# Kernel tuning notes

Hardware: AMD Instinct MI355X
Metric: run time of the kernel (lower is better)

Reference implementation:

```python
import jax, jax.numpy as jnp
import numpy as np

N = 4096          # residues
D = 256           # local feature dim
FACTOR = 2
H = 8             # global heads
DF = D * FACTOR   # 512
DH = DF // H      # 64 per-head dim
NUM_CHAINS = 64
NUM_BATCHES = 8


def index_mean(x, idx, mask, num_segments):
    """Masked segment mean, gathered back to per-element shape.
    x: [N, ...], idx: [N] int, mask: broadcastable to x (0/1)."""
    m = mask.astype(x.dtype)
    xm = x * m
    s = jax.ops.segment_sum(xm, idx, num_segments=num_segments)
    c = jax.ops.segment_sum(jnp.broadcast_to(m, x.shape), idx, num_segments=num_segments)
    mean = s / jnp.maximum(c, 1e-6)
    return mean[idx]


def setup_inputs() -> dict:
    key = jax.random.key(0)
    ks = jax.random.split(key, 12)
    s_in = 1.0 / np.sqrt(D)
    s_mid = 1.0 / np.sqrt(2 * DF)
    return {
        "local": jax.random.normal(ks[0], (N, D), jnp.float32),
        "chain": jax.random.randint(ks[1], (N,), 0, NUM_CHAINS),
        "batch": jax.random.randint(ks[2], (N,), 0, NUM_BATCHES),
        "mask": jax.random.bernoulli(ks[3], 0.9, (N,)),
        "W_key": jax.random.normal(ks[4], (D, DF), jnp.float32) * s_in,
        "b_key": jnp.zeros((DF,), jnp.float32),
        "W_value": jax.random.normal(ks[5], (D, DF), jnp.float32) * s_in,
        "b_value": jnp.zeros((DF,), jnp.float32),
        "W_query": jax.random.normal(ks[6], (D, DF), jnp.float32) * s_in,
        "b_query": jnp.zeros((DF,), jnp.float32),
        "W_bias": jax.random.normal(ks[7], (D, 2 * DF), jnp.float32) * s_in,
        "b_bias": jnp.zeros((2 * DF,), jnp.float32),
        "W_out": jax.random.normal(ks[8], (2 * DF, D), jnp.float32) * s_mid,
    }


def reference(local, chain, batch, mask,
              W_key, b_key, W_value, b_value, W_query, b_query,
              W_bias, b_bias, W_out):
    n = local.shape[0]
    k = jax.nn.gelu(local @ W_key + b_key).reshape(n, H, DH)
    v = (local @ W_value + b_value).reshape(n, H, DH)
    q = jax.nn.gelu(local @ W_query + b_query).reshape(n, H, DH)

    bias = index_mean(local @ W_bias + b_bias, batch, mask[:, None], NUM_BATCHES)

    # outer product key (x) value: [N, H, DH, DH]
    ov = k[:, :, :, None] * v[:, :, None, :]
    m4 = mask[:, None, None, None]
    chain_op = index_mean(ov, chain, m4, NUM_CHAINS)
    batch_op = index_mean(ov, batch, m4, NUM_BATCHES)
    operation = jnp.concatenate((chain_op, batch_op), axis=-2)  # [N, H, 2*DH, DH]

    out = jnp.einsum('bhvk,bhk->bhv', operation, q).reshape(n, -1) + bias
    return out @ W_out
```

## Files before the change

kernel.cpp:

```cpp
#include <hip/hip_runtime.h>
#include <math.h>

#define NN 4096
#define DD 256
#define DFF 512
#define HH 8
#define DHH 64
#define CAP_C 256
#define CAP_B 1024

#define OFF_KB     0
#define OFF_VB     1048576
#define OFF_QB     2097152
#define OFF_ATTNB  3145728
#define OFF_STC    5242880
#define OFF_STB    7340032
#define OFF_BSUM   7602176
#define OFF_CNT    7610368
#define OFF_WQKVT  7610624
#define OFF_WOUTT  7807232
#define OFF_LISTS  7938304
#define OFF_LPART  7987456

typedef __attribute__((ext_vector_type(8))) short bf16x8;
typedef __attribute__((ext_vector_type(4))) float floatx4;

__device__ __forceinline__ float gelu_f(float x) {
    const float c = 0.7978845608028654f;
    float t = tanhf(c * (x + 0.044715f * x * x * x));
    return 0.5f * x * (1.0f + t);
}

__device__ __forceinline__ unsigned short f2b(float f) {
    union { float f; unsigned int u; } v; v.f = f;
    unsigned int r = (v.u + 0x7FFFu + ((v.u >> 16) & 1u)) >> 16;
    return (unsigned short)r;
}

__global__ __launch_bounds__(256) void prep_kernel(
    const float* __restrict__ local,
    const float* __restrict__ Wk, const float* __restrict__ Wv,
    const float* __restrict__ Wq, const float* __restrict__ Wout,
    const int* __restrict__ batch, const int* __restrict__ mask,
    unsigned short* __restrict__ Wqkvt, unsigned short* __restrict__ Woutt,
    float* __restrict__ Lpart, float* __restrict__ zero_base)
{
    const int bid = blockIdx.x, tid = threadIdx.x;
    if (bid < 640) {
        const float* src; unsigned short* dst; int R, C, r0, c0;
        if (bid < 384) {
            int m = bid >> 7, ti = bid & 127;
            src = (m == 0) ? Wk : (m == 1) ? Wv : Wq;
            dst = Wqkvt + (size_t)m * 512 * 256;
            R = 256; C = 512;
            r0 = (ti >> 4) * 32; c0 = (ti & 15) * 32;
        } else {
            int ti = bid - 384;
            src = Wout; dst = Woutt;
            R = 1024; C = 256;
            r0 = (ti >> 3) * 32; c0 = (ti & 7) * 32;
        }
        __shared__ float Tl[32][33];
        int ty = tid >> 3, tx = tid & 7;
        float4 v = *(const float4*)(src + (size_t)(r0 + ty) * C + c0 + tx * 4);
        Tl[tx * 4 + 0][ty] = v.x;
        Tl[tx * 4 + 1][ty] = v.y;
        Tl[tx * 4 + 2][ty] = v.z;
        Tl[tx * 4 + 3][ty] = v.w;
        __syncthreads();
        ushort4 o;
        o.x = f2b(Tl[ty][tx * 4 + 0]);
        o.y = f2b(Tl[ty][tx * 4 + 1]);
        o.z = f2b(Tl[ty][tx * 4 + 2]);
        o.w = f2b(Tl[ty][tx * 4 + 3]);
        *(ushort4*)(dst + (size_t)(c0 + ty) * R + r0 + tx * 4) = o;
    } else if (bid < 704) {
        int p = bid - 640;
        float accl[8] = {};
        int n0 = p * 64;
        for (int r = 0; r < 64; ++r) {
            int n = n0 + r;
            float v = local[(size_t)n * DD + tid];
            int bb = batch[n];
            float vm = mask[n] ? v : 0.0f;
#pragma unroll
            for (int b = 0; b < 8; ++b)
                accl[b] += (bb == b) ? vm : 0.0f;
        }
#pragma unroll
        for (int b = 0; b < 8; ++b)
            Lpart[(size_t)p * 2048 + b * 256 + tid] = accl[b];
    } else {
        float4 z4 = make_float4(0.f, 0.f, 0.f, 0.f);
        for (int i = tid; i < 2112; i += 256)
            ((float4*)zero_base)[i] = z4;
    }
}

__global__ __launch_bounds__(256) void qkv_kernel(
    const float* __restrict__ local, const unsigned short* __restrict__ Wqkvt,
    const float* __restrict__ bk, const float* __restrict__ bv,
    const float* __restrict__ bq, unsigned short* __restrict__ KVQb,
    const int* __restrict__ chain, const int* __restrict__ batch,
    const int* __restrict__ mask, int* __restrict__ cnt,
    int* __restrict__ lists, const float* __restrict__ Lpart,
    const float* __restrict__ Wbias, float* __restrict__ Bsum)
{
    __shared__ __align__(16) char smem[36864];
    const int u = blockIdx.x, tid = threadIdx.x;
    int* cntc_m   = cnt;
    int* cntc_all = cnt + 64;
    int* cntb_m   = cnt + 128;
    int* cntb_all = cnt + 136;
    int* listc_m   = lists;
    int* listc_all = listc_m + 64 * CAP_C;
    int* listb_m   = listc_all + 64 * CAP_C;
    int* listb_all = listb_m + 8 * CAP_B;

    if (u < 384) {
        typedef unsigned short (*t72)[72];
        t72 Asl = (t72)smem;
        t72 Bsl = (t72)(smem + 18432);
        const int wave = tid >> 6, lane = tid & 63;
        const int kq = lane >> 4, la = lane & 15;
        const int cx = u % 12, ry = u / 12;
        const int row0 = ry * 128, cg0 = cx * 128;
        const int wrow = (wave & 1) * 64, wcol = (wave >> 1) * 64;

        floatx4 acc[4][4] = {};
        for (int kk = 0; kk < 256; kk += 64) {
#pragma unroll
            for (int t = 0; t < 4; ++t) {
                int idx = tid + t * 256;
                int rr = idx >> 3, kc = (idx & 7) * 8;
                const float* ap = local + (size_t)(row0 + rr) * DD + kk + kc;
                float4 a0 = *(const float4*)(ap);
                float4 a1 = *(const float4*)(ap + 4);
                ushort4 p0, p1;
                p0.x = f2b(a0.x); p0.y = f2b(a0.y); p0.z = f2b(a0.z); p0.w = f2b(a0.w);
                p1.x = f2b(a1.x); p1.y = f2b(a1.y); p1.z = f2b(a1.z); p1.w = f2b(a1.w);
                *(ushort4*)&Asl[rr][kc] = p0;
                *(ushort4*)&Asl[rr][kc + 4] = p1;
                *(float4*)&Bsl[rr][kc] =
                    *(const float4*)(Wqkvt + (size_t)(cg0 + rr) * DD + kk + kc);
            }
            __syncthreads();
#pragma unroll
            for (int ks = 0; ks < 2; ++ks) {
                bf16x8 af[4], bf[4];
#pragma unroll
                for (int t = 0; t < 4; ++t) {
                    af[t] = *(const bf16x8*)&Asl[wrow + t * 16 + la][ks * 32 + kq * 8];
                    bf[t] = *(const bf16x8*)&Bsl[wcol + t * 16 + la][ks * 32 + kq * 8];
                }
#pragma unroll
                for (int at = 0; at < 4; ++at)
#pragma unroll
                    for (int ct = 0; ct < 4; ++ct)
                        acc[at][ct] = __builtin_amdgcn_mfma_f32_16x16x32_bf16(
                            af[at], bf[ct], acc[at][ct], 0, 0, 0);
            }
            __syncthreads();
        }
        const int sel = cg0 >> 9;
        const int do_gelu = (sel != 1);
        const float* bias = (sel == 0) ? bk : (sel == 1) ? bv : bq;
        unsigned short* C = KVQb + (size_t)sel * (NN * DFF);
#pragma unroll
        for (int ct = 0; ct < 4; ++ct) {
            int colw = (cg0 + wcol + ct * 16 + la) & 511;
            float bb = bias[colw];
#pragma unroll
            for (int at = 0; at < 4; ++at)
#pragma unroll
                for (int i = 0; i < 4; ++i) {
                    int row = row0 + wrow + at * 16 + kq * 4 + i;
                    float o = acc[at][ct][i] + bb;
                    if (do_gelu) o = gelu_f(o);
                    C[(size_t)row * DFF + colw] = f2b(o);
                }
        }
    } else if (u < 400) {
        int* sh = (int*)smem;
        int* hc_m = sh;        int* hc_all = sh + 64;
        int* hb_m = sh + 128;  int* hb_all = sh + 136;
        int* pc_m = sh + 144;  int* pc_all = sh + 208;
        int* pb_m = sh + 272;  int* pb_all = sh + 280;
        if (tid < 64) { hc_m[tid] = 0; hc_all[tid] = 0; }
        if (tid < 8)  { hb_m[tid] = 0; hb_all[tid] = 0; }
        __syncthreads();
        int n = (u - 384) * 256 + tid;
        int c = chain[n], b = batch[n], m = mask[n];
        int rc_all = atomicAdd(&hc_all[c], 1);
        int rb_all = atomicAdd(&hb_all[b], 1);
        int rc_m = -1, rb_m = -1;
        if (m) { rc_m = atomicAdd(&hc_m[c], 1); rb_m = atomicAdd(&hb_m[b], 1); }
        __syncthreads();
        if (tid < 64) {
            pc_all[tid] = atomicAdd(&cntc_all[tid], hc_all[tid]);
            pc_m[tid]   = atomicAdd(&cntc_m[tid],   hc_m[tid]);
        }
        if (tid < 8) {
            pb_all[tid] = atomicAdd(&cntb_all[tid], hb_all[tid]);
            pb_m[tid]   = atomicAdd(&cntb_m[tid],   hb_m[tid]);
        }
        __syncthreads();
        int ia = pc_all[c] + rc_all; if (ia < CAP_C) listc_all[c * CAP_C + ia] = n;
        int ib = pb_all[b] + rb_all; if (ib < CAP_B) listb_all[b * CAP_B + ib] = n;
        if (m) {
            int ja = pc_m[c] + rc_m; if (ja < CAP_C) listc_m[c * CAP_C + ja] = n;
            int jb = pb_m[b] + rb_m; if (jb < CAP_B) listb_m[b * CAP_B + jb] = n;
        }
    } else {
        int t = u - 400;
        const int seg = t >> 3, kz = t & 7;
        float (*Ltmp)[32] = (float(*)[32])smem;
        float* Lk = (float*)(smem + 8192);
        for (int idx = tid; idx < 2048; idx += 256) {
            int p = idx >> 5, k = idx & 31;
            Ltmp[p][k] = Lpart[(size_t)p * 2048 + seg * 256 + kz * 32 + k];
        }
        __syncthreads();
        if (tid < 32) {
            float s = 0.0f;
            for (int p = 0; p < 64; ++p) s += Ltmp[p][tid];
            Lk[tid] = s;
        }
        __syncthreads();
        float4 a4 = make_float4(0, 0, 0, 0);
        for (int k = 0; k < 32; ++k) {
            float l = Lk[k];
            float4 w = *(const float4*)(Wbias + (size_t)(kz * 32 + k) * 1024 + tid * 4);
            a4.x += l * w.x; a4.y += l * w.y; a4.z += l * w.z; a4.w += l * w.w;
        }
        float* o = Bsum + (size_t)seg * 1024 + tid * 4;
        atomicAdd(o + 0, a4.x); atomicAdd(o + 1, a4.y);
        atomicAdd(o + 2, a4.z); atomicAdd(o + 3, a4.w);
    }
}

__global__ __launch_bounds__(256) void mid_kernel(
    const unsigned short* __restrict__ Kb, const unsigned short* __restrict__ Vb,
    const int* __restrict__ listc_m, const int* __restrict__ cntc_m,
    float* __restrict__ STc,
    const int* __restrict__ listb_m, const int* __restrict__ cntb_m,
    float* __restrict__ STb)
{
    const int u = blockIdx.x, tid = threadIdx.x;
    int seg, h, r1, cap;
    const int* list; float* ST;
    if (u < 512) {
        seg = u >> 3; h = u & 7;
        cap = CAP_C; list = listc_m; ST = STc;
        r1 = min(cntc_m[seg], CAP_C);
    } else {
        int t = u - 512;
        seg = t >> 3; h = t & 7;
        cap = CAP_B; list = listb_m; ST = STb;
        r1 = min(cntb_m[seg], CAP_B);
    }

    __shared__ unsigned short Ktl[64][36];
    __shared__ unsigned short Vtl[64][36];
    const int wave = tid >> 6, lane = tid & 63;
    const int la = lane & 15, kq = lane >> 4;

    floatx4 acc4[4] = {};
    for (int g = 0; g < r1; g += 32) {
#pragma unroll
        for (int it = 0; it < 2; ++it) {
            int item = tid + it * 256;
            int nl = item & 31, aq = item >> 5;
            int gg = g + nl;
            ushort4 kz4 = make_ushort4(0, 0, 0, 0);
            ushort4 vz4 = make_ushort4(0, 0, 0, 0);
            if (gg < r1) {
                int nn = list[seg * cap + gg];
                kz4 = *(const ushort4*)(Kb + (size_t)nn * DFF + h * DHH + aq * 4);
                vz4 = *(const ushort4*)(Vb + (size_t)nn * DFF + h * DHH + aq * 4);
            }
            Ktl[aq * 4 + 0][nl] = kz4.x; Ktl[aq * 4 + 1][nl] = kz4.y;
            Ktl[aq * 4 + 2][nl] = kz4.z; Ktl[aq * 4 + 3][nl] = kz4.w;
            Vtl[aq * 4 + 0][nl] = vz4.x; Vtl[aq * 4 + 1][nl] = vz4.y;
            Vtl[aq * 4 + 2][nl] = vz4.z; Vtl[aq * 4 + 3][nl] = vz4.w;
        }
        __syncthreads();
        bf16x8 a = *(const bf16x8*)&Ktl[wave * 16 + la][kq * 8];
#pragma unroll
        for (int bt = 0; bt < 4; ++bt) {
            bf16x8 b = *(const bf16x8*)&Vtl[bt * 16 + la][kq * 8];
            acc4[bt] = __builtin_amdgcn_mfma_f32_16x16x32_bf16(a, b, acc4[bt], 0, 0, 0);
        }
        __syncthreads();
    }

    float* outp = ST + (((size_t)seg * HH + h) << 12);
#pragma unroll
    for (int bt = 0; bt < 4; ++bt)
#pragma unroll
        for (int rg = 0; rg < 4; ++rg) {
            int aa = wave * 16 + kq * 4 + rg;
            int bb2 = bt * 16 + la;
            outp[aa * 64 + bb2] = acc4[bt][rg];
        }
}

__global__ __launch_bounds__(256) void einsum_kernel(
    const float* __restrict__ STc, const int* __restrict__ cntc_m,
    const int* __restrict__ listc_all, const int* __restrict__ cntc_all,
    const float* __restrict__ STb, const int* __restrict__ cntb_m,
    const int* __restrict__ listb_all, const int* __restrict__ cntb_all,
    const unsigned short* __restrict__ Qb, const int* __restrict__ batch,
    const float* __restrict__ Bsum, const float* __restrict__ b_bias,
    unsigned short* __restrict__ attnb)
{
    const int id = blockIdx.x, tid = threadIdx.x;
    int seg, h, outoff, cap, r0, r1;
    const float* ST;
    const int* list;
    float scaleS;
    if (id < 512) {
        seg = id >> 3; h = id & 7; outoff = 0;
        ST = STc; list = listc_all; cap = CAP_C;
        scaleS = 1.0f / fmaxf((float)cntc_m[seg], 1e-6f);
        r0 = 0; r1 = min(cntc_all[seg], CAP_C);
    } else {
        int t = id - 512;
        seg = t >> 6; h = (t >> 3) & 7;
        int z = t & 7;
        outoff = 64;
        ST = STb; list = listb_all; cap = CAP_B;
        scaleS = 1.0f / fmaxf((float)cntb_m[seg], 1e-6f);
        int c = min(cntb_all[seg], CAP_B);
        int chunk = (c + 7) / 8;
        r0 = z * chunk; r1 = min(c, r0 + chunk);
    }

    __shared__ unsigned short Sbl[64][72];
    __shared__ unsigned short Qsl[64][72];
    __shared__ float Bf[8][64];
    __shared__ int nrow[64];
    __shared__ int nbb[64];

    const int wave = tid >> 6, lane = tid & 63;
    const int la = lane & 15, kq = lane >> 4;
    const int colbase = h * 128 + outoff;

    const float* Sg = ST + (((size_t)seg * HH + h) << 12);
#pragma unroll
    for (int i = 0; i < 4; ++i) {
        int e = tid + i * 256;
        float4 v = *(const float4*)(Sg + (size_t)e * 4);
        int a = e >> 4, b = (e & 15) * 4;
        ushort4 o;
        o.x = f2b(v.x * scaleS); o.y = f2b(v.y * scaleS);
        o.z = f2b(v.z * scaleS); o.w = f2b(v.w * scaleS);
        *(ushort4*)&Sbl[a][b] = o;
    }
#pragma unroll
    for (int e = tid; e < 512; e += 256) {
        int bbq = e >> 6, j = e & 63;
        float cm = (float)cntb_m[bbq];
        float inv = 1.0f / fmaxf(cm, 1e-6f);
        int col = colbase + j;
        Bf[bbq][j] = (Bsum[(size_t)bbq * 1024 + col] + cm * b_bias[col]) * inv;
    }
    __syncthreads();

    for (int g = r0; g < r1; g += 64) {
        if (tid < 64) {
            int gg = g + tid;
            int n = (gg < r1) ? list[seg * cap + gg] : -1;
            nrow[tid] = n;
            nbb[tid] = (n >= 0) ? batch[n] : 0;
        }
        __syncthreads();
        {
            int row = tid & 63, pr = tid >> 6;
            int n = nrow[row];
            if (n >= 0) {
#pragma unroll
                for (int it = 0; it < 2; ++it) {
                    int off = (pr + it * 4) * 8;
                    *(float4*)&Qsl[row][off] =
                        *(const float4*)(Qb + (size_t)n * DFF + h * DHH + off);
                }
            }
        }
        __syncthreads();

        floatx4 acc[4] = {};
#pragma unroll
        for (int ks = 0; ks < 2; ++ks) {
            bf16x8 a = *(const bf16x8*)&Qsl[wave * 16 + la][ks * 32 + kq * 8];
#pragma unroll
            for (int ct = 0; ct < 4; ++ct) {
                bf16x8 b = *(const bf16x8*)&Sbl[ct * 16 + la][ks * 32 + kq * 8];
                acc[ct] = __builtin_amdgcn_mfma_f32_16x16x32_bf16(a, b, acc[ct], 0, 0, 0);
            }
        }
#pragma unroll
        for (int ct = 0; ct < 4; ++ct)
#pragma unroll
            for (int rg = 0; rg < 4; ++rg) {
                int rowl = wave * 16 + kq * 4 + rg;
                float bias = Bf[nbb[rowl]][ct * 16 + la];
                Qsl[rowl][ct * 16 + la] = f2b(acc[ct][rg] + bias);
            }
        __syncthreads();
        {
            int row = tid & 63, pr = tid >> 6;
            int n = nrow[row];
            if (n >= 0) {
#pragma unroll
                for (int it = 0; it < 2; ++it) {
                    int off = (pr + it * 4) * 8;
                    *(float4*)(attnb + (size_t)n * 1024 + colbase + off) =
                        *(const float4*)&Qsl[row][off];
                }
            }
        }
        __syncthreads();
    }
}

__global__ __launch_bounds__(256) void mfma_gemm_final(
    const unsigned short* __restrict__ A, const unsigned short* __restrict__ Bt,
    float* __restrict__ out)
{
    const int K = 1024;
    __shared__ unsigned short Asl[32][136];
    __shared__ unsigned short Bsl[64][136];
    const int tid = threadIdx.x;
    const int wave = tid >> 6, lane = tid & 63;
    const int q = lane >> 4, r = lane & 15;
    const int row0 = blockIdx.y * 32, cg0 = blockIdx.x * 64;
    const int wrow = (wave & 1) * 16, wcol = (wave >> 1) * 32;

    floatx4 acc[2] = {};
    for (int kk = 0; kk < K; kk += 128) {
#pragma unroll
        for (int t = 0; t < 2; ++t) {
            int idx = tid + t * 256;
            int rr = idx >> 4, kc = (idx & 15) * 8;
            *(float4*)&Asl[rr][kc] = *(const float4*)(A + (size_t)(row0 + rr) * K + kk + kc);
        }
#pragma unroll
        for (int t = 0; t < 4; ++t) {
            int idx = tid + t * 256;
            int rr = idx >> 4, kc = (idx & 15) * 8;
            *(float4*)&Bsl[rr][kc] = *(const float4*)(Bt + (size_t)(cg0 + rr) * K + kk + kc);
        }
        __syncthreads();
#pragma unroll
        for (int sub = 0; sub < 4; ++sub) {
            bf16x8 a = *(const bf16x8*)&Asl[wrow + r][sub * 32 + q * 8];
#pragma unroll
            for (int c = 0; c < 2; ++c) {
                bf16x8 b = *(const bf16x8*)&Bsl[wcol + c * 16 + r][sub * 32 + q * 8];
                acc[c] = __builtin_amdgcn_mfma_f32_16x16x32_bf16(a, b, acc[c], 0, 0, 0);
            }
        }
        __syncthreads();
    }
#pragma unroll
    for (int c = 0; c < 2; ++c) {
        int col = cg0 + wcol + c * 16 + r;
#pragma unroll
        for (int i = 0; i < 4; ++i) {
            int row = row0 + wrow + q * 4 + i;
            out[(size_t)row * DD + col] = acc[c][i];
        }
    }
}

extern "C" void kernel_launch(void* const* d_in, const int* in_sizes, int n_in,
                              void* d_out, int out_size, void* d_ws, size_t ws_size,
                              hipStream_t stream)
{
    const float* local   = (const float*)d_in[0];
    const int*   chain   = (const int*)d_in[1];
    const int*   batch   = (const int*)d_in[2];
    const int*   mask    = (const int*)d_in[3];
    const float* W_key   = (const float*)d_in[4];
    const float* b_key   = (const float*)d_in[5];
    const float* W_value = (const float*)d_in[6];
    const float* b_value = (const float*)d_in[7];
    const float* W_query = (const float*)d_in[8];
    const float* b_query = (const float*)d_in[9];
    const float* W_bias  = (const float*)d_in[10];
    const float* b_bias  = (const float*)d_in[11];
    const float* W_out   = (const float*)d_in[12];
    float* out = (float*)d_out;

    float* ws = (float*)d_ws;
    unsigned short* Kb    = (unsigned short*)(ws + OFF_KB);
    unsigned short* Vb    = (unsigned short*)(ws + OFF_VB);
    unsigned short* Qb    = (unsigned short*)(ws + OFF_QB);
    unsigned short* attnb = (unsigned short*)(ws + OFF_ATTNB);
    float* STc    = ws + OFF_STC;
    float* STb    = ws + OFF_STB;
    float* Bsum   = ws + OFF_BSUM;
    int*   cnt    = (int*)(ws + OFF_CNT);
    unsigned short* Wqkvt = (unsigned short*)(ws + OFF_WQKVT);
    unsigned short* Woutt = (unsigned short*)(ws + OFF_WOUTT);
    int*   lists  = (int*)(ws + OFF_LISTS);
    float* Lpart  = ws + OFF_LPART;
    int* cntc_m   = cnt;
    int* cntb_m   = cnt + 128;
    int* cntc_all = cnt + 64;
    int* cntb_all = cnt + 136;
    int* listc_m   = lists;
    int* listc_all = listc_m + 64 * CAP_C;
    int* listb_m   = listc_all + 64 * CAP_C;
    int* listb_all = listb_m + 8 * CAP_B;

    dim3 blk(256);

    prep_kernel<<<dim3(705), blk, 0, stream>>>(
        local, W_key, W_value, W_query, W_out, batch, mask,
        Wqkvt, Woutt, Lpart, ws + OFF_BSUM);

    qkv_kernel<<<dim3(464), blk, 0, stream>>>(
        local, Wqkvt, b_key, b_value, b_query, Kb,
        chain, batch, mask, cnt, lists, Lpart, W_bias, Bsum);

    mid_kernel<<<dim3(576), blk, 0, stream>>>(
        Kb, Vb, listc_m, cntc_m, STc, listb_m, cntb_m, STb);

    einsum_kernel<<<dim3(1024), blk, 0, stream>>>(
        STc, cntc_m, listc_all, cntc_all, STb, cntb_m, listb_all, cntb_all,
        Qb, batch, Bsum, b_bias, attnb);

    mfma_gemm_final<<<dim3(4, 128), blk, 0, stream>>>(attnb, Woutt, out);
}
```

Before: 151.6 us.

## Fuse segment outer-product and einsum kernels; pre-convert local to bf16 in prep

Merges mid_kernel and einsum_kernel into one midein_kernel. Each block computes its segment's K^T V summary into registers, scales it and stores it as bf16 in shared memory, then applies it to the queries, so the STc/STb fp32 buffers and one launch are gone. The prep kernel also converts local to bf16 once, so the QKV GEMM loads bf16 tiles directly instead of converting fp32 in every column tile. The trade-off is that batch segments lose the 8-way row split the einsum stage had: only 64 batch blocks, each handling up to 1024 rows, which may create a tail imbalance.

```diff
diff --git a/kernel.cpp b/kernel.cpp
--- a/kernel.cpp
+++ b/kernel.cpp
@@ -13,14 +13,13 @@
 #define OFF_VB     1048576
 #define OFF_QB     2097152
 #define OFF_ATTNB  3145728
-#define OFF_STC    5242880
-#define OFF_STB    7340032
-#define OFF_BSUM   7602176
-#define OFF_CNT    7610368
-#define OFF_WQKVT  7610624
-#define OFF_WOUTT  7807232
-#define OFF_LISTS  7938304
-#define OFF_LPART  7987456
+#define OFF_LOCALB 5242880
+#define OFF_BSUM   5767168
+#define OFF_CNT    5775360
+#define OFF_WQKVT  5775616
+#define OFF_WOUTT  5972224
+#define OFF_LISTS  6103296
+#define OFF_LPART  6152448
 
 typedef __attribute__((ext_vector_type(8))) short bf16x8;
 typedef __attribute__((ext_vector_type(4))) float floatx4;
@@ -43,6 +42,7 @@
     const float* __restrict__ Wq, const float* __restrict__ Wout,
     const int* __restrict__ batch, const int* __restrict__ mask,
     unsigned short* __restrict__ Wqkvt, unsigned short* __restrict__ Woutt,
+    unsigned short* __restrict__ localb,
     float* __restrict__ Lpart, float* __restrict__ zero_base)
 {
     const int bid = blockIdx.x, tid = threadIdx.x;
@@ -90,6 +90,16 @@
 #pragma unroll
         for (int b = 0; b < 8; ++b)
             Lpart[(size_t)p * 2048 + b * 256 + tid] = accl[b];
+    } else if (bid < 1216) {
+        int p = bid - 704;
+        size_t base = (size_t)p * 2048 + tid * 8;
+        float4 a0 = *(const float4*)(local + base);
+        float4 a1 = *(const float4*)(local + base + 4);
+        ushort4 p0, p1;
+        p0.x = f2b(a0.x); p0.y = f2b(a0.y); p0.z = f2b(a0.z); p0.w = f2b(a0.w);
+        p1.x = f2b(a1.x); p1.y = f2b(a1.y); p1.z = f2b(a1.z); p1.w = f2b(a1.w);
+        *(ushort4*)(localb + base) = p0;
+        *(ushort4*)(localb + base + 4) = p1;
     } else {
         float4 z4 = make_float4(0.f, 0.f, 0.f, 0.f);
         for (int i = tid; i < 2112; i += 256)
@@ -98,7 +108,8 @@
 }
 
 __global__ __launch_bounds__(256) void qkv_kernel(
-    const float* __restrict__ local, const unsigned short* __restrict__ Wqkvt,
+    const unsigned short* __restrict__ localb,
+    const unsigned short* __restrict__ Wqkvt,
     const float* __restrict__ bk, const float* __restrict__ bv,
     const float* __restrict__ bq, unsigned short* __restrict__ KVQb,
     const int* __restrict__ chain, const int* __restrict__ batch,
@@ -133,14 +144,8 @@
             for (int t = 0; t < 4; ++t) {
                 int idx = tid + t * 256;
                 int rr = idx >> 3, kc = (idx & 7) * 8;
-                const float* ap = local + (size_t)(row0 + rr) * DD + kk + kc;
-                float4 a0 = *(const float4*)(ap);
-                float4 a1 = *(const float4*)(ap + 4);
-                ushort4 p0, p1;
-                p0.x = f2b(a0.x); p0.y = f2b(a0.y); p0.z = f2b(a0.z); p0.w = f2b(a0.w);
-                p1.x = f2b(a1.x); p1.y = f2b(a1.y); p1.z = f2b(a1.z); p1.w = f2b(a1.w);
-                *(ushort4*)&Asl[rr][kc] = p0;
-                *(ushort4*)&Asl[rr][kc + 4] = p1;
+                *(float4*)&Asl[rr][kc] =
+                    *(const float4*)(localb + (size_t)(row0 + rr) * DD + kk + kc);
                 *(float4*)&Bsl[rr][kc] =
                     *(const float4*)(Wqkvt + (size_t)(cg0 + rr) * DD + kk + kc);
             }
@@ -239,34 +244,54 @@
     }
 }
 
-__global__ __launch_bounds__(256) void mid_kernel(
+__global__ __launch_bounds__(256) void midein_kernel(
     const unsigned short* __restrict__ Kb, const unsigned short* __restrict__ Vb,
-    const int* __restrict__ listc_m, const int* __restrict__ cntc_m,
-    float* __restrict__ STc,
-    const int* __restrict__ listb_m, const int* __restrict__ cntb_m,
-    float* __restrict__ STb)
+    const unsigned short* __restrict__ Qb,
+    const int* __restrict__ cnt, const int* __restrict__ lists,
+    const int* __restrict__ batch,
+    const float* __restrict__ Bsum, const float* __restrict__ b_bias,
+    unsigned short* __restrict__ attnb)
 {
     const int u = blockIdx.x, tid = threadIdx.x;
-    int seg, h, r1, cap;
-    const int* list; float* ST;
+    const int* cntc_m   = cnt;
+    const int* cntc_all = cnt + 64;
+    const int* cntb_m   = cnt + 128;
+    const int* cntb_all = cnt + 136;
+    const int* listc_m   = lists;
+    const int* listc_all = listc_m + 64 * CAP_C;
+    const int* listb_m   = listc_all + 64 * CAP_C;
+    const int* listb_all = listb_m + 8 * CAP_B;
+
+    int seg, h, outoff, cap, rm, ra;
+    const int* list_m; const int* list_a;
     if (u < 512) {
-        seg = u >> 3; h = u & 7;
-        cap = CAP_C; list = listc_m; ST = STc;
-        r1 = min(cntc_m[seg], CAP_C);
+        seg = u >> 3; h = u & 7; outoff = 0; cap = CAP_C;
+        list_m = listc_m; list_a = listc_all;
+        rm = min(cntc_m[seg], CAP_C);
+        ra = min(cntc_all[seg], CAP_C);
     } else {
         int t = u - 512;
-        seg = t >> 3; h = t & 7;
-        cap = CAP_B; list = listb_m; ST = STb;
-        r1 = min(cntb_m[seg], CAP_B);
-    }
+        seg = t >> 3; h = t & 7; outoff = 64; cap = CAP_B;
+        list_m = listb_m; list_a = listb_all;
+        rm = min(cntb_m[seg], CAP_B);
+        ra = min(cntb_all[seg], CAP_B);
+    }
+    float scaleS = 1.0f / fmaxf((float)rm, 1e-6f);
 
     __shared__ unsigned short Ktl[64][36];
     __shared__ unsigned short Vtl[64][36];
+    __shared__ unsigned short Sbl[64][72];
+    __shared__ unsigned short Qsl[64][72];
+    __shared__ float Bf[8][64];
+    __shared__ int nrow[64];
+    __shared__ int nbb[64];
+
     const int wave = tid >> 6, lane = tid & 63;
     const int la = lane & 15, kq = lane >> 4;
+    const int colbase = h * 128 + outoff;
 
     floatx4 acc4[4] = {};
-    for (int g = 0; g < r1; g += 32) {
+    for (int g = 0; g < rm; g += 32) {
 #pragma unroll
         for (int it = 0; it < 2; ++it) {
             int item = tid + it * 256;
@@ -274,8 +299,8 @@
             int gg = g + nl;
             ushort4 kz4 = make_ushort4(0, 0, 0, 0);
             ushort4 vz4 = make_ushort4(0, 0, 0, 0);
-            if (gg < r1) {
-                int nn = list[seg * cap + gg];
+            if (gg < rm) {
+                int nn = list_m[seg * cap + gg];
                 kz4 = *(const ushort4*)(Kb + (size_t)nn * DFF + h * DHH + aq * 4);
                 vz4 = *(const ushort4*)(Vb + (size_t)nn * DFF + h * DHH + aq * 4);
             }
@@ -293,84 +318,28 @@
         }
         __syncthreads();
     }
-
-    float* outp = ST + (((size_t)seg * HH + h) << 12);
 #pragma unroll
     for (int bt = 0; bt < 4; ++bt)
 #pragma unroll
         for (int rg = 0; rg < 4; ++rg) {
             int aa = wave * 16 + kq * 4 + rg;
             int bb2 = bt * 16 + la;
-            outp[aa * 64 + bb2] = acc4[bt][rg];
-        }
-}
-
-__global__ __launch_bounds__(256) void einsum_kernel(
-    const float* __restrict__ STc, const int* __restrict__ cntc_m,
-    const int* __restrict__ listc_all, const int* __restrict__ cntc_all,
-    const float* __restrict__ STb, const int* __restrict__ cntb_m,
-    const int* __restrict__ listb_all, const int* __restrict__ cntb_all,
-    const unsigned short* __restrict__ Qb, const int* __restrict__ batch,
-    const float* __restrict__ Bsum, const float* __restrict__ b_bias,
-    unsigned short* __restrict__ attnb)
-{
-    const int id = blockIdx.x, tid = threadIdx.x;
-    int seg, h, outoff, cap, r0, r1;
-    const float* ST;
-    const int* list;
-    float scaleS;
-    if (id < 512) {
-        seg = id >> 3; h = id & 7; outoff = 0;
-        ST = STc; list = listc_all; cap = CAP_C;
-        scaleS = 1.0f / fmaxf((float)cntc_m[seg], 1e-6f);
-        r0 = 0; r1 = min(cntc_all[seg], CAP_C);
-    } else {
-        int t = id - 512;
-        seg = t >> 6; h = (t >> 3) & 7;
-        int z = t & 7;
-        outoff = 64;
-        ST = STb; list = listb_all; cap = CAP_B;
-        scaleS = 1.0f / fmaxf((float)cntb_m[seg], 1e-6f);
-        int c = min(cntb_all[seg], CAP_B);
-        int chunk = (c + 7) / 8;
-        r0 = z * chunk; r1 = min(c, r0 + chunk);
-    }
-
-    __shared__ unsigned short Sbl[64][72];
-    __shared__ unsigned short Qsl[64][72];
-    __shared__ float Bf[8][64];
-    __shared__ int nrow[64];
-    __shared__ int nbb[64];
-
-    const int wave = tid >> 6, lane = tid & 63;
-    const int la = lane & 15, kq = lane >> 4;
-    const int colbase = h * 128 + outoff;
-
-    const float* Sg = ST + (((size_t)seg * HH + h) << 12);
-#pragma unroll
-    for (int i = 0; i < 4; ++i) {
-        int e = tid + i * 256;
-        float4 v = *(const float4*)(Sg + (size_t)e * 4);
-        int a = e >> 4, b = (e & 15) * 4;
-        ushort4 o;
-        o.x = f2b(v.x * scaleS); o.y = f2b(v.y * scaleS);
-        o.z = f2b(v.z * scaleS); o.w = f2b(v.w * scaleS);
-        *(ushort4*)&Sbl[a][b] = o;
-    }
+            Sbl[aa][bb2] = f2b(acc4[bt][rg] * scaleS);
+        }
 #pragma unroll
     for (int e = tid; e < 512; e += 256) {
         int bbq = e >> 6, j = e & 63;
-        float cm = (float)cntb_m[bbq];
+        float cm = (float)min(cntb_m[bbq], CAP_B);
         float inv = 1.0f / fmaxf(cm, 1e-6f);
         int col = colbase + j;
         Bf[bbq][j] = (Bsum[(size_t)bbq * 1024 + col] + cm * b_bias[col]) * inv;
     }
     __syncthreads();
 
-    for (int g = r0; g < r1; g += 64) {
+    for (int g = 0; g < ra; g += 64) {
         if (tid < 64) {
             int gg = g + tid;
-            int n = (gg < r1) ? list[seg * cap + gg] : -1;
+            int n = (gg < ra) ? list_a[seg * cap + gg] : -1;
             nrow[tid] = n;
             nbb[tid] = (n >= 0) ? batch[n] : 0;
         }
@@ -494,43 +463,30 @@
     float* out = (float*)d_out;
 
     float* ws = (float*)d_ws;
-    unsigned short* Kb    = (unsigned short*)(ws + OFF_KB);
-    unsigned short* Vb    = (unsigned short*)(ws + OFF_VB);
-    unsigned short* Qb    = (unsigned short*)(ws + OFF_QB);
-    unsigned short* attnb = (unsigned short*)(ws + OFF_ATTNB);
-    float* STc    = ws + OFF_STC;
-    float* STb    = ws + OFF_STB;
+    unsigned short* Kb     = (unsigned short*)(ws + OFF_KB);
+    unsigned short* Vb     = (unsigned short*)(ws + OFF_VB);
+    unsigned short* Qb     = (unsigned short*)(ws + OFF_QB);
+    unsigned short* attnb  = (unsigned short*)(ws + OFF_ATTNB);
+    unsigned short* localb = (unsigned short*)(ws + OFF_LOCALB);
     float* Bsum   = ws + OFF_BSUM;
     int*   cnt    = (int*)(ws + OFF_CNT);
     unsigned short* Wqkvt = (unsigned short*)(ws + OFF_WQKVT);
     unsigned short* Woutt = (unsigned short*)(ws + OFF_WOUTT);
     int*   lists  = (int*)(ws + OFF_LISTS);
     float* Lpart  = ws + OFF_LPART;
-    int* cntc_m   = cnt;
-    int* cntb_m   = cnt + 128;
-    int* cntc_all = cnt + 64;
-    int* cntb_all = cnt + 136;
-    int* listc_m   = lists;
-    int* listc_all = listc_m + 64 * CAP_C;
-    int* listb_m   = listc_all + 64 * CAP_C;
-    int* listb_all = listb_m + 8 * CAP_B;
 
     dim3 blk(256);
 
-    prep_kernel<<<dim3(705), blk, 0, stream>>>(
+    prep_kernel<<<dim3(1217), blk, 0, stream>>>(
         local, W_key, W_value, W_query, W_out, batch, mask,
-        Wqkvt, Woutt, Lpart, ws + OFF_BSUM);
+        Wqkvt, Woutt, localb, Lpart, ws + OFF_BSUM);
 
     qkv_kernel<<<dim3(464), blk, 0, stream>>>(
-        local, Wqkvt, b_key, b_value, b_query, Kb,
+        localb, Wqkvt, b_key, b_value, b_query, Kb,
         chain, batch, mask, cnt, lists, Lpart, W_bias, Bsum);
 
-    mid_kernel<<<dim3(576), blk, 0, stream>>>(
-        Kb, Vb, listc_m, cntc_m, STc, listb_m, cntb_m, STb);
-
-    einsum_kernel<<<dim3(1024), blk, 0, stream>>>(
-        STc, cntc_m, listc_all, cntc_all, STb, cntb_m, listb_all, cntb_all,
-        Qb, batch, Bsum, b_bias, attnb);
+    midein_kernel<<<dim3(576), blk, 0, stream>>>(
+        Kb, Vb, Qb, cnt, lists, batch, Bsum, b_bias, attnb);
 
     mfma_gemm_final<<<dim3(4, 128), blk, 0, stream>>>(attnb, Woutt, out);
 }
```

After: 162.7 us. 1.07x slower.
